# Optimization experiments

Hardware: AMD Instinct MI355X
Metric: run time of the kernel (lower is better)

## Reference

```python
import jax, jax.numpy as jnp
import numpy as np


def setup_inputs() -> dict:
    key = jax.random.key(0)
    k1, k2 = jax.random.split(key)
    x = jax.random.normal(k1, (32, 64, 64, 64), dtype=jnp.float32)  # [B, C, H, W]
    limit = 3 ** 0.5
    embeddings = jax.random.uniform(k2, (64, 512), dtype=jnp.float32,
                                    minval=-limit, maxval=limit)  # [D, K]
    return {"x": x, "embeddings": embeddings}


def reference(x, embeddings):
    B, D, H, W = x.shape
    # NCHW -> NHWC -> [N, D]
    flat_x = jnp.transpose(x, (0, 2, 3, 1)).reshape(-1, D)
    distances = (
        jnp.sum(flat_x ** 2, axis=1, keepdims=True)
        - 2.0 * flat_x @ embeddings
        + jnp.sum(embeddings ** 2, axis=0, keepdims=True)
    )
    encoding_indices = jnp.argmin(distances, axis=1)  # [N]
    # gather codebook rows: embeddings.T is [K, D]
    quantized = embeddings.T[encoding_indices].reshape(B, H, W, D)
    quantized = jnp.transpose(quantized, (0, 3, 1, 2))  # back to NCHW
    commitment_loss = jnp.mean((x - jax.lax.stop_gradient(quantized)) ** 2)
    # straight-through estimator
    quantized_ste = x + jax.lax.stop_gradient(quantized - x)
    return quantized_ste, commitment_loss, encoding_indices.reshape(B, -1)
```

## Files before the change

### kernel.cpp

```cpp
#include <hip/hip_runtime.h>

#define D      64
#define K      512
#define Q_OFF  0
#define L_OFF  8388608
#define I_OFF  8388609

#define WS_ET    0
#define WS_EN    32768
#define WS_ENH   33280
#define WS_PART  33792
#define WS_BH    36864
#define WS_BL    53248

#define SEL_SCALE 16384.0f
#define SEL_BIAS  (160.0f * 16384.0f)

typedef __attribute__((ext_vector_type(8))) short short8;
typedef __attribute__((ext_vector_type(4))) float f32x4;

static __device__ __forceinline__ unsigned short f2bf(float f) {
    unsigned u = __float_as_uint(f);
    u += 0x7fffu + ((u >> 16) & 1u);
    return (unsigned short)(u >> 16);
}
static __device__ __forceinline__ float bf2f(unsigned short h) {
    return __uint_as_float(((unsigned)h) << 16);
}

__device__ __forceinline__ void gload_lds16(const float* g, float* l) {
    __builtin_amdgcn_global_load_lds(
        (const __attribute__((address_space(1))) unsigned int*)g,
        (__attribute__((address_space(3))) unsigned int*)l, 16, 0, 0);
}

__global__ __launch_bounds__(256) void vq_prep(const float* __restrict__ E,
                                               float* __restrict__ ws) {
    int g = blockIdx.x * 256 + threadIdx.x;
    int t = g >> 6, lane = g & 63;
    int col = lane & 15, kg = lane >> 4;
    int code = t * 16 + col;
    short8* bhp = (short8*)(ws + WS_BH);
    short8* blp = (short8*)(ws + WS_BL);
#pragma unroll
    for (int s = 0; s < 2; ++s) {
        short8 h, l;
#pragma unroll
        for (int j = 0; j < 8; ++j) {
            int k = s * 32 + kg * 8 + j;
            float v = -E[k * K + code];
            unsigned short hb = f2bf(v);
            h[j] = (short)hb;
            l[j] = (short)f2bf(v - bf2f(hb));
        }
        bhp[(t * 2 + s) * 64 + lane] = h;
        blp[(t * 2 + s) * 64 + lane] = l;
    }
    if (g < K) {
        float nsq = 0.f;
#pragma unroll 8
        for (int d = 0; d < D; ++d) {
            float v = E[d * K + g];
            ws[WS_ET + g * D + d] = v;
            nsq = fmaf(v, v, nsq);
        }
        ws[WS_EN + g]  = nsq;
        ws[WS_ENH + g] = 0.5f * nsq;
    }
}

__device__ __forceinline__ float dot32(const float* __restrict__ er,
                                       const float* __restrict__ xv) {
    const float4* e4 = (const float4*)er;
    float a0 = 0.f, a1 = 0.f, a2 = 0.f, a3 = 0.f;
#pragma unroll
    for (int q = 0; q < 8; ++q) {
        float4 e = e4[q];
        a0 = fmaf(xv[4*q+0], e.x, a0);
        a1 = fmaf(xv[4*q+1], e.y, a1);
        a2 = fmaf(xv[4*q+2], e.z, a2);
        a3 = fmaf(xv[4*q+3], e.w, a3);
    }
    return (a0 + a1) + (a2 + a3);
}

__global__ __launch_bounds__(128, 4) void vq_fused(const float* __restrict__ x,
                                                   float* __restrict__ ws,
                                                   float* __restrict__ out,
                                                   float* __restrict__ partial) {
    __shared__ float sbuf[3][1024];
    __shared__ float senh[512];
    __shared__ unsigned sc[64];
    __shared__ float2 sdot[2][64];

    const int tid = threadIdx.x, w = tid >> 6, lane = tid & 63;
    const int col = lane & 15, rowg = lane >> 4;
    const int pixw = blockIdx.x * 64 + w * 32;

    const float* bh = ws + WS_BH;
    const float* bl = ws + WS_BL;

    gload_lds16(ws + WS_ENH + tid * 4, senh + tid * 4);
    gload_lds16(bh + tid * 4,       sbuf[0] + tid * 4);
    gload_lds16(bl + tid * 4,       sbuf[0] + 512 + tid * 4);
    gload_lds16(bh + 512 + tid * 4, sbuf[1] + tid * 4);
    gload_lds16(bl + 512 + tid * 4, sbuf[1] + 512 + tid * 4);

    short8 ah[2][2], al[2][2];
#pragma unroll
    for (int mt = 0; mt < 2; ++mt) {
        int pix = pixw + mt * 16 + col;
        const float* xp = x + ((size_t)(pix >> 12) << 18) + (pix & 4095);
#pragma unroll
        for (int s = 0; s < 2; ++s) {
            short8 h, l;
#pragma unroll
            for (int j = 0; j < 8; ++j) {
                float v = xp[(size_t)(s * 32 + rowg * 8 + j) << 12];
                unsigned short hb = f2bf(v);
                h[j] = (short)hb;
                l[j] = (short)f2bf(v - bf2f(hb));
            }
            ah[mt][s] = h; al[mt][s] = l;
        }
    }

    unsigned m1[2][4], m2[2][4];
#pragma unroll
    for (int mt = 0; mt < 2; ++mt)
#pragma unroll
        for (int r = 0; r < 4; ++r) { m1[mt][r] = 0xFFFFFFFFu; m2[mt][r] = 0xFFFFFFFFu; }

    int cbuf = 0;
    for (int c = 0; c < 32; ++c) {
        if (c < 31) asm volatile("s_waitcnt vmcnt(2)" ::: "memory");
        else        asm volatile("s_waitcnt vmcnt(0)" ::: "memory");
        __builtin_amdgcn_s_barrier();
        __builtin_amdgcn_sched_barrier(0);

        if (c + 2 < 32) {
            int sb2 = (cbuf >= 1) ? cbuf - 1 : 2;
            const float* sh = bh + (c + 2) * 512;
            const float* sl = bl + (c + 2) * 512;
            gload_lds16(sh + tid * 4, sbuf[sb2] + tid * 4);
            gload_lds16(sl + tid * 4, sbuf[sb2] + 512 + tid * 4);
        }

        const short8* sb = (const short8*)sbuf[cbuf];
        const float ev = senh[c * 16 + col];
        const unsigned codev = (unsigned)(c * 16 + col);

        short8 cbh0 = sb[lane];
        short8 cbh1 = sb[64 + lane];
        short8 cbl0 = sb[128 + lane];
        short8 cbl1 = sb[192 + lane];

        f32x4 acc0 = { ev, ev, ev, ev };
        f32x4 acc1 = { ev, ev, ev, ev };
        __builtin_amdgcn_s_setprio(1);
        acc0 = __builtin_amdgcn_mfma_f32_16x16x32_bf16(ah[0][0], cbh0, acc0, 0, 0, 0);
        acc1 = __builtin_amdgcn_mfma_f32_16x16x32_bf16(ah[1][0], cbh0, acc1, 0, 0, 0);
        acc0 = __builtin_amdgcn_mfma_f32_16x16x32_bf16(al[0][0], cbh0, acc0, 0, 0, 0);
        acc1 = __builtin_amdgcn_mfma_f32_16x16x32_bf16(al[1][0], cbh0, acc1, 0, 0, 0);
        acc0 = __builtin_amdgcn_mfma_f32_16x16x32_bf16(ah[0][0], cbl0, acc0, 0, 0, 0);
        acc1 = __builtin_amdgcn_mfma_f32_16x16x32_bf16(ah[1][0], cbl0, acc1, 0, 0, 0);
        acc0 = __builtin_amdgcn_mfma_f32_16x16x32_bf16(ah[0][1], cbh1, acc0, 0, 0, 0);
        acc1 = __builtin_amdgcn_mfma_f32_16x16x32_bf16(ah[1][1], cbh1, acc1, 0, 0, 0);
        acc0 = __builtin_amdgcn_mfma_f32_16x16x32_bf16(al[0][1], cbh1, acc0, 0, 0, 0);
        acc1 = __builtin_amdgcn_mfma_f32_16x16x32_bf16(al[1][1], cbh1, acc1, 0, 0, 0);
        acc0 = __builtin_amdgcn_mfma_f32_16x16x32_bf16(ah[0][1], cbl1, acc0, 0, 0, 0);
        acc1 = __builtin_amdgcn_mfma_f32_16x16x32_bf16(ah[1][1], cbl1, acc1, 0, 0, 0);
        __builtin_amdgcn_s_setprio(0);

#pragma unroll
        for (int r = 0; r < 4; ++r) {
            unsigned p0 = (((unsigned)fmaf(acc0[r], SEL_SCALE, SEL_BIAS)) << 9) + codev;
            m2[0][r] = min(m2[0][r], max(m1[0][r], p0));
            m1[0][r] = min(m1[0][r], p0);
            unsigned p1 = (((unsigned)fmaf(acc1[r], SEL_SCALE, SEL_BIAS)) << 9) + codev;
            m2[1][r] = min(m2[1][r], max(m1[1][r], p1));
            m1[1][r] = min(m1[1][r], p1);
        }

        cbuf = (cbuf == 2) ? 0 : cbuf + 1;
    }

#pragma unroll
    for (int mt = 0; mt < 2; ++mt)
#pragma unroll
        for (int r = 0; r < 4; ++r) {
            unsigned v1 = m1[mt][r], v2 = m2[mt][r];
#pragma unroll
            for (int m = 1; m < 16; m <<= 1) {
                unsigned o1 = (unsigned)__shfl_xor((int)v1, m, 16);
                unsigned o2 = (unsigned)__shfl_xor((int)v2, m, 16);
                v2 = min(max(v1, o1), min(v2, o2));
                v1 = min(v1, o1);
            }
            if (col == r)
                sc[w * 32 + mt * 16 + rowg * 4 + r] = (v1 & 511u) | ((v2 & 511u) << 16);
        }
    __syncthreads();

    const float* ET = ws + WS_ET;
    const float* EN = ws + WS_EN;
    const int pl   = tid & 63;
    const int half = tid >> 6;
    const int n    = blockIdx.x * 64 + pl;
    const int b    = n >> 12;
    const int hw   = n & 4095;

    unsigned pk = sc[pl];
    int c1 = (int)(pk & 0xffffu), c2 = (int)(pk >> 16);

    const float* xp2 = x + ((size_t)b << 18) + ((size_t)half << 17) + hw;
    float xv2[32];
#pragma unroll
    for (int d = 0; d < 32; ++d) xv2[d] = xp2[(size_t)d << 12];

    float dp1 = dot32(ET + (c1 << 6) + half * 32, xv2);
    float dp2 = dot32(ET + (c2 << 6) + half * 32, xv2);
    sdot[half][pl] = make_float2(dp1, dp2);
    __syncthreads();
    float2 lo = sdot[0][pl], hi = sdot[1][pl];
    float d1 = fmaf(-2.f, lo.x + hi.x, EN[c1]);
    float d2 = fmaf(-2.f, lo.y + hi.y, EN[c2]);
    bool sw = (d2 < d1) || (d2 == d1 && c2 < c1);
    int bestk = sw ? c2 : c1;

    if (!half) out[I_OFF + n] = (float)bestk;

    const float* qv = ET + (bestk << 6) + half * 32;
    float* op = out + Q_OFF + ((size_t)b << 18) + ((size_t)half << 17) + hw;
    float lsum = 0.f;
#pragma unroll
    for (int d = 0; d < 32; ++d) {
        float qd = qv[d];
        op[(size_t)d << 12] = qd;
        float diff = xv2[d] - qd;
        lsum = fmaf(diff, diff, lsum);
    }

#pragma unroll
    for (int off = 32; off > 0; off >>= 1)
        lsum += __shfl_down(lsum, off, 64);
    __shared__ float wsum[2];
    if ((tid & 63) == 0) wsum[tid >> 6] = lsum;
    __syncthreads();
    if (tid == 0)
        partial[blockIdx.x] = wsum[0] + wsum[1];
}

__global__ __launch_bounds__(256) void vq_final(const float* __restrict__ partial,
                                                float* __restrict__ out) {
    int t = threadIdx.x;
    float s = 0.f;
#pragma unroll
    for (int i = 0; i < 8; ++i) s += partial[t + 256 * i];
#pragma unroll
    for (int off = 32; off > 0; off >>= 1)
        s += __shfl_down(s, off, 64);
    __shared__ float wsum[4];
    if ((t & 63) == 0) wsum[t >> 6] = s;
    __syncthreads();
    if (t == 0)
        out[L_OFF] = ((wsum[0] + wsum[1]) + (wsum[2] + wsum[3])) * (1.f / 8388608.f);
}

extern "C" void kernel_launch(void* const* d_in, const int* in_sizes, int n_in,
                              void* d_out, int out_size, void* d_ws, size_t ws_size,
                              hipStream_t stream) {
    const float* x = (const float*)d_in[0];
    const float* E = (const float*)d_in[1];
    float* out = (float*)d_out;
    float* ws  = (float*)d_ws;

    hipLaunchKernelGGL(vq_prep,  dim3(8),    dim3(256), 0, stream, E, ws);
    hipLaunchKernelGGL(vq_fused, dim3(2048), dim3(128), 0, stream, x, ws, out, ws + WS_PART);
    hipLaunchKernelGGL(vq_final, dim3(1),    dim3(256), 0, stream, ws + WS_PART, out);
}
```

Baseline: 62.15 us.

## Halve per-block pixel tile, double grid, simplify codebook pipeline to double buffer

Each block now handles 32 pixels instead of 64 (one 16-pixel MFMA tile per wave), doubling the grid to 4096 blocks and raising launch bounds to 8 waves per SIMD. The triple-buffered async codebook pipeline with explicit vmcnt waits becomes a double buffer with a full __syncthreads per chunk, and the half-norm bias is read from global instead of LDS. The epilogue splits channels four ways across threads. This lowers register and LDS use to raise occupancy, at the cost of reloading the codebook twice as often overall and adding a block barrier every iteration.

```diff
diff --git a/kernel.cpp b/kernel.cpp
--- a/kernel.cpp
+++ b/kernel.cpp
@@ -10,8 +10,8 @@
 #define WS_EN    32768
 #define WS_ENH   33280
 #define WS_PART  33792
-#define WS_BH    36864
-#define WS_BL    53248
+#define WS_BH    40960
+#define WS_BL    57344
 
 #define SEL_SCALE 16384.0f
 #define SEL_BIAS  (160.0f * 16384.0f)
@@ -69,12 +69,12 @@
     }
 }
 
-__device__ __forceinline__ float dot32(const float* __restrict__ er,
+__device__ __forceinline__ float dot16(const float* __restrict__ er,
                                        const float* __restrict__ xv) {
     const float4* e4 = (const float4*)er;
     float a0 = 0.f, a1 = 0.f, a2 = 0.f, a3 = 0.f;
 #pragma unroll
-    for (int q = 0; q < 8; ++q) {
+    for (int q = 0; q < 4; ++q) {
         float4 e = e4[q];
         a0 = fmaf(xv[4*q+0], e.x, a0);
         a1 = fmaf(xv[4*q+1], e.y, a1);
@@ -84,32 +84,29 @@
     return (a0 + a1) + (a2 + a3);
 }
 
-__global__ __launch_bounds__(128, 4) void vq_fused(const float* __restrict__ x,
+__global__ __launch_bounds__(128, 8) void vq_fused(const float* __restrict__ x,
                                                    float* __restrict__ ws,
                                                    float* __restrict__ out,
                                                    float* __restrict__ partial) {
-    __shared__ float sbuf[3][1024];
-    __shared__ float senh[512];
-    __shared__ unsigned sc[64];
-    __shared__ float2 sdot[2][64];
+    __shared__ float sbuf[2][1024];
+    __shared__ unsigned sc[32];
+    __shared__ float2 sdot[4][32];
+    __shared__ float wsum[2];
 
     const int tid = threadIdx.x, w = tid >> 6, lane = tid & 63;
     const int col = lane & 15, rowg = lane >> 4;
-    const int pixw = blockIdx.x * 64 + w * 32;
-
-    const float* bh = ws + WS_BH;
-    const float* bl = ws + WS_BL;
-
-    gload_lds16(ws + WS_ENH + tid * 4, senh + tid * 4);
-    gload_lds16(bh + tid * 4,       sbuf[0] + tid * 4);
-    gload_lds16(bl + tid * 4,       sbuf[0] + 512 + tid * 4);
-    gload_lds16(bh + 512 + tid * 4, sbuf[1] + tid * 4);
-    gload_lds16(bl + 512 + tid * 4, sbuf[1] + 512 + tid * 4);
-
-    short8 ah[2][2], al[2][2];
-#pragma unroll
-    for (int mt = 0; mt < 2; ++mt) {
-        int pix = pixw + mt * 16 + col;
+    const int pixw = blockIdx.x * 32 + w * 16;
+
+    const float* bh    = ws + WS_BH;
+    const float* bl    = ws + WS_BL;
+    const float* enh_g = ws + WS_ENH;
+
+    gload_lds16(bh + tid * 4, sbuf[0] + tid * 4);
+    gload_lds16(bl + tid * 4, sbuf[0] + 512 + tid * 4);
+
+    short8 ah[2], al[2];
+    {
+        int pix = pixw + col;
         const float* xp = x + ((size_t)(pix >> 12) << 18) + (pix & 4095);
 #pragma unroll
         for (int s = 0; s < 2; ++s) {
@@ -121,33 +118,27 @@
                 h[j] = (short)hb;
                 l[j] = (short)f2bf(v - bf2f(hb));
             }
-            ah[mt][s] = h; al[mt][s] = l;
-        }
-    }
-
-    unsigned m1[2][4], m2[2][4];
-#pragma unroll
-    for (int mt = 0; mt < 2; ++mt)
-#pragma unroll
-        for (int r = 0; r < 4; ++r) { m1[mt][r] = 0xFFFFFFFFu; m2[mt][r] = 0xFFFFFFFFu; }
-
-    int cbuf = 0;
+            ah[s] = h; al[s] = l;
+        }
+    }
+
+    unsigned m1[4], m2[4];
+#pragma unroll
+    for (int r = 0; r < 4; ++r) { m1[r] = 0xFFFFFFFFu; m2[r] = 0xFFFFFFFFu; }
+
+    __syncthreads();
+
     for (int c = 0; c < 32; ++c) {
-        if (c < 31) asm volatile("s_waitcnt vmcnt(2)" ::: "memory");
-        else        asm volatile("s_waitcnt vmcnt(0)" ::: "memory");
-        __builtin_amdgcn_s_barrier();
-        __builtin_amdgcn_sched_barrier(0);
-
-        if (c + 2 < 32) {
-            int sb2 = (cbuf >= 1) ? cbuf - 1 : 2;
-            const float* sh = bh + (c + 2) * 512;
-            const float* sl = bl + (c + 2) * 512;
-            gload_lds16(sh + tid * 4, sbuf[sb2] + tid * 4);
-            gload_lds16(sl + tid * 4, sbuf[sb2] + 512 + tid * 4);
-        }
-
-        const short8* sb = (const short8*)sbuf[cbuf];
-        const float ev = senh[c * 16 + col];
+        if (c + 1 < 32) {
+            const float* sh = bh + (c + 1) * 512;
+            const float* sl = bl + (c + 1) * 512;
+            float* db = sbuf[(c + 1) & 1];
+            gload_lds16(sh + tid * 4, db + tid * 4);
+            gload_lds16(sl + tid * 4, db + 512 + tid * 4);
+        }
+
+        const short8* sb = (const short8*)sbuf[c & 1];
+        const float ev = enh_g[c * 16 + col];
         const unsigned codev = (unsigned)(c * 16 + col);
 
         short8 cbh0 = sb[lane];
@@ -155,86 +146,74 @@
         short8 cbl0 = sb[128 + lane];
         short8 cbl1 = sb[192 + lane];
 
-        f32x4 acc0 = { ev, ev, ev, ev };
-        f32x4 acc1 = { ev, ev, ev, ev };
+        f32x4 acc = { ev, ev, ev, ev };
         __builtin_amdgcn_s_setprio(1);
-        acc0 = __builtin_amdgcn_mfma_f32_16x16x32_bf16(ah[0][0], cbh0, acc0, 0, 0, 0);
-        acc1 = __builtin_amdgcn_mfma_f32_16x16x32_bf16(ah[1][0], cbh0, acc1, 0, 0, 0);
-        acc0 = __builtin_amdgcn_mfma_f32_16x16x32_bf16(al[0][0], cbh0, acc0, 0, 0, 0);
-        acc1 = __builtin_amdgcn_mfma_f32_16x16x32_bf16(al[1][0], cbh0, acc1, 0, 0, 0);
-        acc0 = __builtin_amdgcn_mfma_f32_16x16x32_bf16(ah[0][0], cbl0, acc0, 0, 0, 0);
-        acc1 = __builtin_amdgcn_mfma_f32_16x16x32_bf16(ah[1][0], cbl0, acc1, 0, 0, 0);
-        acc0 = __builtin_amdgcn_mfma_f32_16x16x32_bf16(ah[0][1], cbh1, acc0, 0, 0, 0);
-        acc1 = __builtin_amdgcn_mfma_f32_16x16x32_bf16(ah[1][1], cbh1, acc1, 0, 0, 0);
-        acc0 = __builtin_amdgcn_mfma_f32_16x16x32_bf16(al[0][1], cbh1, acc0, 0, 0, 0);
-        acc1 = __builtin_amdgcn_mfma_f32_16x16x32_bf16(al[1][1], cbh1, acc1, 0, 0, 0);
-        acc0 = __builtin_amdgcn_mfma_f32_16x16x32_bf16(ah[0][1], cbl1, acc0, 0, 0, 0);
-        acc1 = __builtin_amdgcn_mfma_f32_16x16x32_bf16(ah[1][1], cbl1, acc1, 0, 0, 0);
+        acc = __builtin_amdgcn_mfma_f32_16x16x32_bf16(ah[0], cbh0, acc, 0, 0, 0);
+        acc = __builtin_amdgcn_mfma_f32_16x16x32_bf16(al[0], cbh0, acc, 0, 0, 0);
+        acc = __builtin_amdgcn_mfma_f32_16x16x32_bf16(ah[0], cbl0, acc, 0, 0, 0);
+        acc = __builtin_amdgcn_mfma_f32_16x16x32_bf16(ah[1], cbh1, acc, 0, 0, 0);
+        acc = __builtin_amdgcn_mfma_f32_16x16x32_bf16(al[1], cbh1, acc, 0, 0, 0);
+        acc = __builtin_amdgcn_mfma_f32_16x16x32_bf16(ah[1], cbl1, acc, 0, 0, 0);
         __builtin_amdgcn_s_setprio(0);
 
 #pragma unroll
         for (int r = 0; r < 4; ++r) {
-            unsigned p0 = (((unsigned)fmaf(acc0[r], SEL_SCALE, SEL_BIAS)) << 9) + codev;
-            m2[0][r] = min(m2[0][r], max(m1[0][r], p0));
-            m1[0][r] = min(m1[0][r], p0);
-            unsigned p1 = (((unsigned)fmaf(acc1[r], SEL_SCALE, SEL_BIAS)) << 9) + codev;
-            m2[1][r] = min(m2[1][r], max(m1[1][r], p1));
-            m1[1][r] = min(m1[1][r], p1);
-        }
-
-        cbuf = (cbuf == 2) ? 0 : cbuf + 1;
-    }
-
-#pragma unroll
-    for (int mt = 0; mt < 2; ++mt)
-#pragma unroll
-        for (int r = 0; r < 4; ++r) {
-            unsigned v1 = m1[mt][r], v2 = m2[mt][r];
-#pragma unroll
-            for (int m = 1; m < 16; m <<= 1) {
-                unsigned o1 = (unsigned)__shfl_xor((int)v1, m, 16);
-                unsigned o2 = (unsigned)__shfl_xor((int)v2, m, 16);
-                v2 = min(max(v1, o1), min(v2, o2));
-                v1 = min(v1, o1);
-            }
-            if (col == r)
-                sc[w * 32 + mt * 16 + rowg * 4 + r] = (v1 & 511u) | ((v2 & 511u) << 16);
-        }
+            unsigned p0 = (((unsigned)fmaf(acc[r], SEL_SCALE, SEL_BIAS)) << 9) + codev;
+            m2[r] = min(m2[r], max(m1[r], p0));
+            m1[r] = min(m1[r], p0);
+        }
+
+        __syncthreads();
+    }
+
+#pragma unroll
+    for (int r = 0; r < 4; ++r) {
+        unsigned v1 = m1[r], v2 = m2[r];
+#pragma unroll
+        for (int m = 1; m < 16; m <<= 1) {
+            unsigned o1 = (unsigned)__shfl_xor((int)v1, m, 16);
+            unsigned o2 = (unsigned)__shfl_xor((int)v2, m, 16);
+            v2 = min(max(v1, o1), min(v2, o2));
+            v1 = min(v1, o1);
+        }
+        if (col == r)
+            sc[w * 16 + rowg * 4 + r] = (v1 & 511u) | ((v2 & 511u) << 16);
+    }
     __syncthreads();
 
     const float* ET = ws + WS_ET;
     const float* EN = ws + WS_EN;
-    const int pl   = tid & 63;
-    const int half = tid >> 6;
-    const int n    = blockIdx.x * 64 + pl;
+    const int pl   = tid & 31;
+    const int part = tid >> 5;
+    const int n    = blockIdx.x * 32 + pl;
     const int b    = n >> 12;
     const int hw   = n & 4095;
 
     unsigned pk = sc[pl];
     int c1 = (int)(pk & 0xffffu), c2 = (int)(pk >> 16);
 
-    const float* xp2 = x + ((size_t)b << 18) + ((size_t)half << 17) + hw;
-    float xv2[32];
-#pragma unroll
-    for (int d = 0; d < 32; ++d) xv2[d] = xp2[(size_t)d << 12];
-
-    float dp1 = dot32(ET + (c1 << 6) + half * 32, xv2);
-    float dp2 = dot32(ET + (c2 << 6) + half * 32, xv2);
-    sdot[half][pl] = make_float2(dp1, dp2);
-    __syncthreads();
-    float2 lo = sdot[0][pl], hi = sdot[1][pl];
-    float d1 = fmaf(-2.f, lo.x + hi.x, EN[c1]);
-    float d2 = fmaf(-2.f, lo.y + hi.y, EN[c2]);
+    const float* xp2 = x + ((size_t)b << 18) + ((size_t)part << 16) + hw;
+    float xv2[16];
+#pragma unroll
+    for (int d = 0; d < 16; ++d) xv2[d] = xp2[(size_t)d << 12];
+
+    float dp1 = dot16(ET + (c1 << 6) + part * 16, xv2);
+    float dp2 = dot16(ET + (c2 << 6) + part * 16, xv2);
+    sdot[part][pl] = make_float2(dp1, dp2);
+    __syncthreads();
+    float2 q0 = sdot[0][pl], q1 = sdot[1][pl], q2 = sdot[2][pl], q3 = sdot[3][pl];
+    float d1 = fmaf(-2.f, (q0.x + q1.x) + (q2.x + q3.x), EN[c1]);
+    float d2 = fmaf(-2.f, (q0.y + q1.y) + (q2.y + q3.y), EN[c2]);
     bool sw = (d2 < d1) || (d2 == d1 && c2 < c1);
     int bestk = sw ? c2 : c1;
 
-    if (!half) out[I_OFF + n] = (float)bestk;
-
-    const float* qv = ET + (bestk << 6) + half * 32;
-    float* op = out + Q_OFF + ((size_t)b << 18) + ((size_t)half << 17) + hw;
+    if (part == 0) out[I_OFF + n] = (float)bestk;
+
+    const float* qv = ET + (bestk << 6) + part * 16;
+    float* op = out + Q_OFF + ((size_t)b << 18) + ((size_t)part << 16) + hw;
     float lsum = 0.f;
 #pragma unroll
-    for (int d = 0; d < 32; ++d) {
+    for (int d = 0; d < 16; ++d) {
         float qd = qv[d];
         op[(size_t)d << 12] = qd;
         float diff = xv2[d] - qd;
@@ -244,7 +223,6 @@
 #pragma unroll
     for (int off = 32; off > 0; off >>= 1)
         lsum += __shfl_down(lsum, off, 64);
-    __shared__ float wsum[2];
     if ((tid & 63) == 0) wsum[tid >> 6] = lsum;
     __syncthreads();
     if (tid == 0)
@@ -256,7 +234,7 @@
     int t = threadIdx.x;
     float s = 0.f;
 #pragma unroll
-    for (int i = 0; i < 8; ++i) s += partial[t + 256 * i];
+    for (int i = 0; i < 16; ++i) s += partial[t + 256 * i];
 #pragma unroll
     for (int off = 32; off > 0; off >>= 1)
         s += __shfl_down(s, off, 64);
@@ -276,6 +254,6 @@
     float* ws  = (float*)d_ws;
 
     hipLaunchKernelGGL(vq_prep,  dim3(8),    dim3(256), 0, stream, E, ws);
-    hipLaunchKernelGGL(vq_fused, dim3(2048), dim3(128), 0, stream, x, ws, out, ws + WS_PART);
+    hipLaunchKernelGGL(vq_fused, dim3(4096), dim3(128), 0, stream, x, ws, out, ws + WS_PART);
     hipLaunchKernelGGL(vq_final, dim3(1),    dim3(256), 0, stream, ws + WS_PART, out);
 }
```

Result: no change. 61.64 us, median of 3 (-0.8%).
